# Performance work log

Measured on AMD Instinct MI355X. Metric: run time of the kernel, lower is better.

## Reference

```python
import jax, jax.numpy as jnp
import numpy as np

N_NODES = 100000
N_EDGES = 3200000
IN_DIM = 256
OUT_DIM = 128


def setup_inputs() -> dict:
    key = jax.random.key(0)
    k_x, k_w, k_r, k_c, k_v = jax.random.split(key, 5)
    X = jax.random.normal(k_x, (N_NODES, IN_DIM), dtype=jnp.float32)
    # kaiming_normal on [in, out]: fan computed along dim 1 -> std = sqrt(2/out)
    weight = jax.random.normal(k_w, (IN_DIM, OUT_DIM), dtype=jnp.float32) * np.sqrt(2.0 / OUT_DIM)
    bias = jnp.zeros((OUT_DIM,), dtype=jnp.float32)
    adj_rows = jax.random.randint(k_r, (N_EDGES,), 0, N_NODES, dtype=jnp.int32)
    adj_cols = jax.random.randint(k_c, (N_EDGES,), 0, N_NODES, dtype=jnp.int32)
    adj_vals = jax.random.uniform(k_v, (N_EDGES,), dtype=jnp.float32)
    return {"X": X, "weight": weight, "bias": bias,
            "adj_rows": adj_rows, "adj_cols": adj_cols, "adj_vals": adj_vals}


def reference(X, weight, bias, adj_rows, adj_cols, adj_vals):
    # support = X @ W  -> [N, out]
    support = jnp.matmul(X, weight)
    # SpMM: output[r] = sum_e vals[e] * support[cols[e]] for edges with rows[e]==r
    messages = adj_vals[:, None] * support[adj_cols]          # [E, out]
    output = jax.ops.segment_sum(messages, adj_rows, num_segments=N_NODES)
    return output + bias
```

## Files before the change

### kernel.cpp

```cpp
#include <hip/hip_runtime.h>

#define N_NODES 100000
#define N_EDGES 3200000
#define IN_DIM  256
#define OUT_DIM 128

#define CB      256
#define NCB     391
#define NB2     256
#define CHUNK2  12500
#define NQ4     (CHUNK2 / 4)
#define SCAN_N  (NCB * NB2)
#define SCAN_BS 1024
#define SCAN_NB ((SCAN_N + SCAN_BS - 1) / SCAN_BS)

#define GBM 128

typedef __attribute__((ext_vector_type(8))) short bf16x8;
typedef __attribute__((ext_vector_type(4))) float f32x4;
typedef unsigned int u32x2 __attribute__((ext_vector_type(2)));
typedef unsigned int u32x4 __attribute__((ext_vector_type(4)));

__device__ __forceinline__ unsigned short f2bf(float x) {
    unsigned u = __float_as_uint(x);
    unsigned r = (u + 0x7FFFu + ((u >> 16) & 1u)) >> 16;
    return (unsigned short)r;
}
__device__ __forceinline__ unsigned cvtpk_bf16(float lo, float hi) {
    unsigned r;
    asm("v_cvt_pk_bf16_f32 %0, %1, %2" : "=v"(r) : "v"(lo), "v"(hi));
    return r;
}
__device__ __forceinline__ float bflo(unsigned d) { return __uint_as_float(d << 16); }
__device__ __forceinline__ float bfhi(unsigned d) { return __uint_as_float(d & 0xFFFF0000u); }

__global__ __launch_bounds__(256) void wtrans_kernel(const float* __restrict__ W,
                                                     unsigned short* __restrict__ WT) {
    const int n = blockIdx.x;
    const int k = threadIdx.x;
    WT[(size_t)n * IN_DIM + k] = f2bf(W[(size_t)k * OUT_DIM + n]);
}

__global__ __launch_bounds__(256) void gemm_mfma(const float* __restrict__ X,
                                                 const unsigned short* __restrict__ WT,
                                                 unsigned short* __restrict__ SH) {
    __shared__ char lds[32768];
    char* ldsX = lds;
    char* ldsW = lds + 16384;

    const int t    = threadIdx.x;
    const int row0 = blockIdx.x * GBM;
    const int w    = t >> 6;
    const int l    = t & 63;
    const int r16  = l & 15;
    const int kg   = l >> 4;

    f32x4 acc[2][8];
#pragma unroll
    for (int mr = 0; mr < 2; ++mr)
#pragma unroll
        for (int nc = 0; nc < 8; ++nc) acc[mr][nc] = (f32x4)(0.f);

    const int srow = t >> 1;
    const int sseg = t & 1;

    for (int k0 = 0; k0 < IN_DIM; k0 += 64) {
        {
            int grow = row0 + srow;
            bool live = grow < N_NODES;
            const float4* xp = (const float4*)(X + (size_t)(live ? grow : 0) * IN_DIM + k0 + sseg * 32);
#pragma unroll
            for (int c = 0; c < 4; ++c) {
                uint4 wv = make_uint4(0, 0, 0, 0);
                if (live) {
                    float4 fa = xp[c * 2], fb = xp[c * 2 + 1];
                    wv.x = cvtpk_bf16(fa.x, fa.y);
                    wv.y = cvtpk_bf16(fa.z, fa.w);
                    wv.z = cvtpk_bf16(fb.x, fb.y);
                    wv.w = cvtpk_bf16(fb.z, fb.w);
                }
                int byte = srow * 128 + (sseg * 32 + c * 8) * 2;
                byte ^= (srow & 7) << 4;
                *(uint4*)(ldsX + byte) = wv;
            }
            const uint4* wp = (const uint4*)(WT + (size_t)srow * IN_DIM + k0 + sseg * 32);
#pragma unroll
            for (int c = 0; c < 4; ++c) {
                uint4 wv = wp[c];
                int byte = srow * 128 + (sseg * 32 + c * 8) * 2;
                byte ^= (srow & 7) << 4;
                *(uint4*)(ldsW + byte) = wv;
            }
        }
        __syncthreads();

#pragma unroll
        for (int ks = 0; ks < 64; ks += 32) {
            bf16x8 af[2], bfr[8];
#pragma unroll
            for (int mr = 0; mr < 2; ++mr) {
                int row  = w * 32 + mr * 16 + r16;
                int byte = row * 128 + (ks + kg * 8) * 2;
                byte ^= (row & 7) << 4;
                af[mr] = *(const bf16x8*)(ldsX + byte);
            }
#pragma unroll
            for (int nc = 0; nc < 8; ++nc) {
                int n    = nc * 16 + r16;
                int byte = n * 128 + (ks + kg * 8) * 2;
                byte ^= (n & 7) << 4;
                bfr[nc] = *(const bf16x8*)(ldsW + byte);
            }
#pragma unroll
            for (int mr = 0; mr < 2; ++mr)
#pragma unroll
                for (int nc = 0; nc < 8; ++nc)
                    acc[mr][nc] = __builtin_amdgcn_mfma_f32_16x16x32_bf16(af[mr], bfr[nc], acc[mr][nc], 0, 0, 0);
        }
        __syncthreads();
    }

#pragma unroll
    for (int mr = 0; mr < 2; ++mr)
#pragma unroll
        for (int j = 0; j < 4; ++j) {
            int grow = row0 + w * 32 + mr * 16 + kg * 4 + j;
            if (grow < N_NODES) {
#pragma unroll
                for (int nc = 0; nc < 8; ++nc)
                    SH[(size_t)grow * OUT_DIM + nc * 16 + r16] = f2bf(acc[mr][nc][j]);
            }
        }
}

__global__ __launch_bounds__(1024) void pA_hist(const int* __restrict__ rows,
                                                int* __restrict__ gcounts) {
    __shared__ int hist[NCB];
    const int b = blockIdx.x, t = threadIdx.x;
    for (int k = t; k < NCB; k += 1024) hist[k] = 0;
    __syncthreads();
    const int4* r4 = (const int4*)(rows + b * CHUNK2);
    for (int q = t; q < NQ4; q += 1024) {
        int4 r = r4[q];
        atomicAdd(&hist[r.x >> 8], 1);
        atomicAdd(&hist[r.y >> 8], 1);
        atomicAdd(&hist[r.z >> 8], 1);
        atomicAdd(&hist[r.w >> 8], 1);
    }
    __syncthreads();
    for (int k = t; k < NCB; k += 1024) gcounts[k * NB2 + b] = hist[k];
}

__global__ __launch_bounds__(256) void scan1_kernel(int* __restrict__ data,
                                                    int* __restrict__ bsums) {
    __shared__ int tsum[256];
    const int t    = threadIdx.x;
    const int base = blockIdx.x * SCAN_BS + t * 4;
    int v[4];
#pragma unroll
    for (int j = 0; j < 4; ++j) {
        int idx = base + j;
        v[j] = (idx < SCAN_N) ? data[idx] : 0;
    }
    tsum[t] = v[0] + v[1] + v[2] + v[3];
    __syncthreads();
    for (int off = 1; off < 256; off <<= 1) {
        int x = (t >= off) ? tsum[t - off] : 0;
        __syncthreads();
        tsum[t] += x;
        __syncthreads();
    }
    int run = (t == 0) ? 0 : tsum[t - 1];
#pragma unroll
    for (int j = 0; j < 4; ++j) {
        int idx = base + j;
        if (idx < SCAN_N) data[idx] = run;
        run += v[j];
    }
    if (t == 255) bsums[blockIdx.x] = tsum[255];
}

__global__ __launch_bounds__(64) void scan2_kernel(int* __restrict__ bsums) {
    const int lane = threadIdx.x & 63;
    const int base = lane * 4;
    int v[4];
    int s = 0;
#pragma unroll
    for (int j = 0; j < 4; ++j) {
        int idx = base + j;
        v[j] = (idx < SCAN_NB) ? bsums[idx] : 0;
        s += v[j];
    }
    for (int off = 1; off < 64; off <<= 1) {
        int x = __shfl_up(s, off);
        if (lane >= off) s += x;
    }
    int run = s - v[0] - v[1] - v[2] - v[3];
#pragma unroll
    for (int j = 0; j < 4; ++j) {
        int idx = base + j;
        if (idx < SCAN_NB) bsums[idx] = run;
        run += v[j];
    }
}

__global__ __launch_bounds__(256) void scan3_kernel(int* __restrict__ data,
                                                    const int* __restrict__ bsums) {
    int i = blockIdx.x * 256 + threadIdx.x;
    if (i < SCAN_N) data[i] += bsums[i / SCAN_BS];
}

__global__ __launch_bounds__(1024) void pA_scatter(const int* __restrict__ rows,
                                                   const int* __restrict__ cols,
                                                   const float* __restrict__ vals,
                                                   const int* __restrict__ pscan,
                                                   uint2* __restrict__ sorted) {
    __shared__ int cursor[NCB];
    const int b = blockIdx.x, t = threadIdx.x;
    for (int k = t; k < NCB; k += 1024) cursor[k] = pscan[k * NB2 + b];
    __syncthreads();
    const int4*   r4 = (const int4*)(rows + b * CHUNK2);
    const int4*   c4 = (const int4*)(cols + b * CHUNK2);
    const float4* v4 = (const float4*)(vals + b * CHUNK2);
    for (int q = t; q < NQ4; q += 1024) {
        int4   r = r4[q];
        int4   c = c4[q];
        float4 v = v4[q];
#define PUT(rr, cc, vv)                                                        \
        {                                                                      \
            int pos = atomicAdd(&cursor[(rr) >> 8], 1);                        \
            sorted[pos] = make_uint2(__float_as_uint(vv),                      \
                                     ((unsigned)((rr) & (CB - 1)) << 17) | (unsigned)(cc)); \
        }
        PUT(r.x, c.x, v.x)
        PUT(r.y, c.y, v.y)
        PUT(r.z, c.z, v.z)
        PUT(r.w, c.w, v.w)
#undef PUT
    }
}

__global__ __launch_bounds__(1024) void pB_sort(const uint2* __restrict__ sortedA,
                                                const int* __restrict__ pscan,
                                                unsigned* __restrict__ sorted2,
                                                int* __restrict__ rstart2) {
    __shared__ int cnt[CB];
    __shared__ int cur[CB];
    __shared__ int sbuf[2][CB];
    const int cb = blockIdx.x, t = threadIdx.x;
    const int beg  = pscan[cb * NB2];
    const int gend = (cb == NCB - 1) ? N_EDGES : pscan[(cb + 1) * NB2];

    if (t < CB) cnt[t] = 0;
    __syncthreads();

    for (int i = beg + t; i < gend; i += 1024)
        atomicAdd(&cnt[(sortedA[i].y >> 17) & (CB - 1)], 1);
    __syncthreads();

    if (t < CB) sbuf[0][t] = cnt[t];
    __syncthreads();
    int p = 0;
    for (int off = 1; off < CB; off <<= 1) {
        if (t < CB) sbuf[p ^ 1][t] = sbuf[p][t] + ((t >= off) ? sbuf[p][t - off] : 0);
        __syncthreads();
        p ^= 1;
    }
    if (t < CB) {
        int excl = (t == 0) ? 0 : sbuf[p][t - 1];
        int gi   = cb * CB + t;
        if (gi <= N_NODES) rstart2[gi] = beg + excl;
        cur[t] = beg + excl;
    }
    __syncthreads();

    for (int i = beg + t; i < gend; i += 1024) {
        uint2 m  = sortedA[i];
        int   rl = (int)((m.y >> 17) & (CB - 1));
        int  pos = atomicAdd(&cur[rl], 1);
        float v  = __uint_as_float(m.x);
        unsigned vq = (unsigned)__float2int_rn(v * 32767.0f);
        sorted2[pos] = (m.y & 0x1FFFFu) | (vq << 17);
    }
}

__global__ __launch_bounds__(256) void p6_rowsum(const int* __restrict__ rstart2,
                                                 const unsigned* __restrict__ meta,
                                                 const unsigned short* __restrict__ SH,
                                                 const float* __restrict__ bias,
                                                 float* __restrict__ out) {
    const int wid  = (blockIdx.x * 256 + threadIdx.x) >> 6;
    const int lane = threadIdx.x & 63;
    if (wid >= N_NODES) return;

    const int beg = rstart2[wid];
    const int end = rstart2[wid + 1];
    const int qg  = lane >> 4;
    const int ql  = lane & 15;

    float a0 = 0.f, a1 = 0.f, a2 = 0.f, a3 = 0.f, a4 = 0.f, a5 = 0.f, a6 = 0.f, a7 = 0.f;

#define DEQ(mm) ((float)((mm) >> 17) * (1.0f / 32767.0f))
#define GATHER(mm) (*((const u32x4*)(SH + (size_t)((mm) & 0x1FFFFu) * OUT_DIM) + ql))
#define ACC8(vv, gg)                                          \
    {                                                         \
        a0 += (vv) * bflo((gg).x); a1 += (vv) * bfhi((gg).x); \
        a2 += (vv) * bflo((gg).y); a3 += (vv) * bfhi((gg).y); \
        a4 += (vv) * bflo((gg).z); a5 += (vv) * bfhi((gg).z); \
        a6 += (vv) * bflo((gg).w); a7 += (vv) * bfhi((gg).w); \
    }

    int i = beg;
    for (; i + 8 <= end; i += 8) {
        unsigned m0 = meta[i + qg];
        unsigned m1 = meta[i + 4 + qg];
        u32x4 g0 = GATHER(m0);
        u32x4 g1 = GATHER(m1);
        float v0 = DEQ(m0);
        float v1 = DEQ(m1);
        ACC8(v0, g0)
        ACC8(v1, g1)
    }
    for (; i < end; i += 4) {
        int      idx  = i + qg;
        int      cidx = (idx < end) ? idx : (end - 1);
        unsigned m    = meta[cidx];
        float    v    = (idx < end) ? DEQ(m) : 0.f;
        u32x4    g    = GATHER(m);
        ACC8(v, g)
    }
#undef ACC8
#undef GATHER
#undef DEQ

    a0 += __shfl_xor(a0, 16); a1 += __shfl_xor(a1, 16); a2 += __shfl_xor(a2, 16); a3 += __shfl_xor(a3, 16);
    a4 += __shfl_xor(a4, 16); a5 += __shfl_xor(a5, 16); a6 += __shfl_xor(a6, 16); a7 += __shfl_xor(a7, 16);
    a0 += __shfl_xor(a0, 32); a1 += __shfl_xor(a1, 32); a2 += __shfl_xor(a2, 32); a3 += __shfl_xor(a3, 32);
    a4 += __shfl_xor(a4, 32); a5 += __shfl_xor(a5, 32); a6 += __shfl_xor(a6, 32); a7 += __shfl_xor(a7, 32);

    if (lane < 16) {
        const float4* bp = (const float4*)bias + ql * 2;
        float4 b0 = bp[0], b1 = bp[1];
        f32x4 o0 = {a0 + b0.x, a1 + b0.y, a2 + b0.z, a3 + b0.w};
        f32x4 o1 = {a4 + b1.x, a5 + b1.y, a6 + b1.z, a7 + b1.w};
        f32x4* orow = (f32x4*)(out + (size_t)wid * OUT_DIM) + ql * 2;
        __builtin_nontemporal_store(o0, orow);
        __builtin_nontemporal_store(o1, orow + 1);
    }
}

extern "C" void kernel_launch(void* const* d_in, const int* in_sizes, int n_in,
                              void* d_out, int out_size, void* d_ws, size_t ws_size,
                              hipStream_t stream) {
    const float* X    = (const float*)d_in[0];
    const float* W    = (const float*)d_in[1];
    const float* bias = (const float*)d_in[2];
    const int*   rows = (const int*)d_in[3];
    const int*   cols = (const int*)d_in[4];
    const float* vals = (const float*)d_in[5];
    float* out = (float*)d_out;

    char* ws = (char*)d_ws;
    unsigned short* SH      = (unsigned short*)ws;
    uint2*          sortedA = (uint2*)(ws + 25600000);
    unsigned*       sorted2 = (unsigned*)(ws + 51200000);
    int*            pscan   = (int*)(ws + 64000000);
    int*            rstart2 = (int*)(ws + 64400384);
    int*            bsums   = (int*)(ws + 64800768);
    unsigned short* WT      = (unsigned short*)(ws + 64801280);

    hipLaunchKernelGGL(wtrans_kernel, dim3(OUT_DIM), dim3(IN_DIM), 0, stream, W, WT);
    hipLaunchKernelGGL(gemm_mfma, dim3((N_NODES + GBM - 1) / GBM), dim3(256), 0, stream,
                       X, WT, SH);
    hipLaunchKernelGGL(pA_hist, dim3(NB2), dim3(1024), 0, stream, rows, pscan);
    hipLaunchKernelGGL(scan1_kernel, dim3(SCAN_NB), dim3(256), 0, stream, pscan, bsums);
    hipLaunchKernelGGL(scan2_kernel, dim3(1), dim3(64), 0, stream, bsums);
    hipLaunchKernelGGL(scan3_kernel, dim3((SCAN_N + 255) / 256), dim3(256), 0, stream,
                       pscan, bsums);
    hipLaunchKernelGGL(pA_scatter, dim3(NB2), dim3(1024), 0, stream,
                       rows, cols, vals, pscan, sortedA);
    hipLaunchKernelGGL(pB_sort, dim3(NCB), dim3(1024), 0, stream,
                       sortedA, pscan, sorted2, rstart2);
    hipLaunchKernelGGL(p6_rowsum, dim3((N_NODES + 3) / 4), dim3(256), 0, stream,
                       rstart2, sorted2, SH, bias, out);
}
```

Measured before the change: 201.6 us.

## Compute per-row counts in histogram pass and prefetch metadata in rowsum

The histogram kernel now also builds a per-row edge count with global atomics, so the second-stage sort no longer rereads all of sortedA to count rows. The rowsum gather loop is restructured to software-prefetch the next metadata words before doing the current gathers. The cost is 3.2M extra global atomics on a 100k-entry array plus an extra zeroing kernel launch, which could offset the saved pass over sortedA.

```diff
diff --git a/kernel.cpp b/kernel.cpp
--- a/kernel.cpp
+++ b/kernel.cpp
@@ -39,6 +39,11 @@
     const int n = blockIdx.x;
     const int k = threadIdx.x;
     WT[(size_t)n * IN_DIM + k] = f2bf(W[(size_t)k * OUT_DIM + n]);
+}
+
+__global__ __launch_bounds__(256) void zero_rowcnt(int* __restrict__ rowcnt) {
+    int i = blockIdx.x * 256 + threadIdx.x;
+    if (i < SCAN_N) rowcnt[i] = 0;
 }
 
 __global__ __launch_bounds__(256) void gemm_mfma(const float* __restrict__ X,
@@ -134,7 +139,8 @@
 }
 
 __global__ __launch_bounds__(1024) void pA_hist(const int* __restrict__ rows,
-                                                int* __restrict__ gcounts) {
+                                                int* __restrict__ gcounts,
+                                                int* __restrict__ rowcnt) {
     __shared__ int hist[NCB];
     const int b = blockIdx.x, t = threadIdx.x;
     for (int k = t; k < NCB; k += 1024) hist[k] = 0;
@@ -146,6 +152,10 @@
         atomicAdd(&hist[r.y >> 8], 1);
         atomicAdd(&hist[r.z >> 8], 1);
         atomicAdd(&hist[r.w >> 8], 1);
+        atomicAdd(&rowcnt[r.x], 1);
+        atomicAdd(&rowcnt[r.y], 1);
+        atomicAdd(&rowcnt[r.z], 1);
+        atomicAdd(&rowcnt[r.w], 1);
     }
     __syncthreads();
     for (int k = t; k < NCB; k += 1024) gcounts[k * NB2 + b] = hist[k];
@@ -242,23 +252,19 @@
 
 __global__ __launch_bounds__(1024) void pB_sort(const uint2* __restrict__ sortedA,
                                                 const int* __restrict__ pscan,
+                                                const int* __restrict__ rowcnt,
                                                 unsigned* __restrict__ sorted2,
                                                 int* __restrict__ rstart2) {
-    __shared__ int cnt[CB];
     __shared__ int cur[CB];
     __shared__ int sbuf[2][CB];
     const int cb = blockIdx.x, t = threadIdx.x;
     const int beg  = pscan[cb * NB2];
     const int gend = (cb == NCB - 1) ? N_EDGES : pscan[(cb + 1) * NB2];
 
-    if (t < CB) cnt[t] = 0;
-    __syncthreads();
-
-    for (int i = beg + t; i < gend; i += 1024)
-        atomicAdd(&cnt[(sortedA[i].y >> 17) & (CB - 1)], 1);
-    __syncthreads();
-
-    if (t < CB) sbuf[0][t] = cnt[t];
+    if (t < CB) {
+        int gi = cb * CB + t;
+        sbuf[0][t] = (gi < N_NODES) ? rowcnt[gi] : 0;
+    }
     __syncthreads();
     int p = 0;
     for (int off = 1; off < CB; off <<= 1) {
@@ -311,15 +317,31 @@
     }
 
     int i = beg;
-    for (; i + 8 <= end; i += 8) {
-        unsigned m0 = meta[i + qg];
-        unsigned m1 = meta[i + 4 + qg];
-        u32x4 g0 = GATHER(m0);
-        u32x4 g1 = GATHER(m1);
-        float v0 = DEQ(m0);
-        float v1 = DEQ(m1);
+    unsigned pm0 = 0, pm1 = 0;
+    if (i + 8 <= end) {
+        pm0 = meta[i + qg];
+        pm1 = meta[i + 4 + qg];
+    }
+    for (; i + 16 <= end; i += 8) {
+        unsigned nm0 = meta[i + 8 + qg];
+        unsigned nm1 = meta[i + 12 + qg];
+        u32x4 g0 = GATHER(pm0);
+        u32x4 g1 = GATHER(pm1);
+        float v0 = DEQ(pm0);
+        float v1 = DEQ(pm1);
         ACC8(v0, g0)
         ACC8(v1, g1)
+        pm0 = nm0;
+        pm1 = nm1;
+    }
+    if (i + 8 <= end) {
+        u32x4 g0 = GATHER(pm0);
+        u32x4 g1 = GATHER(pm1);
+        float v0 = DEQ(pm0);
+        float v1 = DEQ(pm1);
+        ACC8(v0, g0)
+        ACC8(v1, g1)
+        i += 8;
     }
     for (; i < end; i += 4) {
         int      idx  = i + qg;
@@ -366,13 +388,15 @@
     unsigned*       sorted2 = (unsigned*)(ws + 51200000);
     int*            pscan   = (int*)(ws + 64000000);
     int*            rstart2 = (int*)(ws + 64400384);
-    int*            bsums   = (int*)(ws + 64800768);
-    unsigned short* WT      = (unsigned short*)(ws + 64801280);
-
+    int*            rowcnt  = (int*)(ws + 64800768);
+    int*            bsums   = (int*)(ws + 65201152);
+    unsigned short* WT      = (unsigned short*)(ws + 65201664);
+
+    hipLaunchKernelGGL(zero_rowcnt, dim3((SCAN_N + 255) / 256), dim3(256), 0, stream, rowcnt);
     hipLaunchKernelGGL(wtrans_kernel, dim3(OUT_DIM), dim3(IN_DIM), 0, stream, W, WT);
     hipLaunchKernelGGL(gemm_mfma, dim3((N_NODES + GBM - 1) / GBM), dim3(256), 0, stream,
                        X, WT, SH);
-    hipLaunchKernelGGL(pA_hist, dim3(NB2), dim3(1024), 0, stream, rows, pscan);
+    hipLaunchKernelGGL(pA_hist, dim3(NB2), dim3(1024), 0, stream, rows, pscan, rowcnt);
     hipLaunchKernelGGL(scan1_kernel, dim3(SCAN_NB), dim3(256), 0, stream, pscan, bsums);
     hipLaunchKernelGGL(scan2_kernel, dim3(1), dim3(64), 0, stream, bsums);
     hipLaunchKernelGGL(scan3_kernel, dim3((SCAN_N + 255) / 256), dim3(256), 0, stream,
@@ -380,7 +404,7 @@
     hipLaunchKernelGGL(pA_scatter, dim3(NB2), dim3(1024), 0, stream,
                        rows, cols, vals, pscan, sortedA);
     hipLaunchKernelGGL(pB_sort, dim3(NCB), dim3(1024), 0, stream,
-                       sortedA, pscan, sorted2, rstart2);
+                       sortedA, pscan, rowcnt, sorted2, rstart2);
     hipLaunchKernelGGL(p6_rowsum, dim3((N_NODES + 3) / 4), dim3(256), 0, stream,
                        rstart2, sorted2, SH, bias, out);
 }
```

Measured after the change: 323.5 us. 60.4% more time.

## Replace LDS-staged GEMM with direct global-to-register MFMA fragment loads

Applied to the files above, without the earlier changes.

Rewrites the dense X@W GEMM so each wavefront loads its A fragments from X and its B fragments from the transposed bf16 weight directly into registers, with no LDS staging or __syncthreads. Blocks grow to 512 threads (8 waves of 32 rows each) and the grid is sized to NCB blocks. This removes LDS traffic and barrier stalls, but every wave now reloads the full weight matrix from global/L2 and the A loads are less coalesced (16 rows per fragment, 32-byte segments).

```diff
diff --git a/kernel.cpp b/kernel.cpp
--- a/kernel.cpp
+++ b/kernel.cpp
@@ -14,12 +14,12 @@
 #define SCAN_BS 1024
 #define SCAN_NB ((SCAN_N + SCAN_BS - 1) / SCAN_BS)
 
-#define GBM 128
-
 typedef __attribute__((ext_vector_type(8))) short bf16x8;
 typedef __attribute__((ext_vector_type(4))) float f32x4;
 typedef unsigned int u32x2 __attribute__((ext_vector_type(2)));
 typedef unsigned int u32x4 __attribute__((ext_vector_type(4)));
+
+union pkcast { u32x4 u; bf16x8 h; };
 
 __device__ __forceinline__ unsigned short f2bf(float x) {
     unsigned u = __float_as_uint(x);
@@ -41,94 +41,53 @@
     WT[(size_t)n * IN_DIM + k] = f2bf(W[(size_t)k * OUT_DIM + n]);
 }
 
-__global__ __launch_bounds__(256) void gemm_mfma(const float* __restrict__ X,
-                                                 const unsigned short* __restrict__ WT,
-                                                 unsigned short* __restrict__ SH) {
-    __shared__ char lds[32768];
-    char* ldsX = lds;
-    char* ldsW = lds + 16384;
-
+__global__ __launch_bounds__(512) void gemm_direct(const float* __restrict__ X,
+                                                   const unsigned short* __restrict__ WT,
+                                                   unsigned short* __restrict__ SH) {
     const int t    = threadIdx.x;
-    const int row0 = blockIdx.x * GBM;
     const int w    = t >> 6;
     const int l    = t & 63;
     const int r16  = l & 15;
     const int kg   = l >> 4;
+    const int row0 = (blockIdx.x * 8 + w) * 32;
 
     f32x4 acc[2][8];
 #pragma unroll
-    for (int mr = 0; mr < 2; ++mr)
-#pragma unroll
-        for (int nc = 0; nc < 8; ++nc) acc[mr][nc] = (f32x4)(0.f);
-
-    const int srow = t >> 1;
-    const int sseg = t & 1;
-
-    for (int k0 = 0; k0 < IN_DIM; k0 += 64) {
-        {
-            int grow = row0 + srow;
-            bool live = grow < N_NODES;
-            const float4* xp = (const float4*)(X + (size_t)(live ? grow : 0) * IN_DIM + k0 + sseg * 32);
-#pragma unroll
-            for (int c = 0; c < 4; ++c) {
-                uint4 wv = make_uint4(0, 0, 0, 0);
-                if (live) {
-                    float4 fa = xp[c * 2], fb = xp[c * 2 + 1];
-                    wv.x = cvtpk_bf16(fa.x, fa.y);
-                    wv.y = cvtpk_bf16(fa.z, fa.w);
-                    wv.z = cvtpk_bf16(fb.x, fb.y);
-                    wv.w = cvtpk_bf16(fb.z, fb.w);
-                }
-                int byte = srow * 128 + (sseg * 32 + c * 8) * 2;
-                byte ^= (srow & 7) << 4;
-                *(uint4*)(ldsX + byte) = wv;
-            }
-            const uint4* wp = (const uint4*)(WT + (size_t)srow * IN_DIM + k0 + sseg * 32);
-#pragma unroll
-            for (int c = 0; c < 4; ++c) {
-                uint4 wv = wp[c];
-                int byte = srow * 128 + (sseg * 32 + c * 8) * 2;
-                byte ^= (srow & 7) << 4;
-                *(uint4*)(ldsW + byte) = wv;
-            }
+    for (int m = 0; m < 2; ++m)
+#pragma unroll
+        for (int nc = 0; nc < 8; ++nc) acc[m][nc] = (f32x4)(0.f);
+
+#pragma unroll
+    for (int k0 = 0; k0 < IN_DIM; k0 += 32) {
+        bf16x8 af[2];
+#pragma unroll
+        for (int m = 0; m < 2; ++m) {
+            int row = row0 + m * 16 + r16;
+            if (row >= N_NODES) row = N_NODES - 1;
+            const float4* ap = (const float4*)(X + (size_t)row * IN_DIM + k0 + kg * 8);
+            float4 fa = ap[0], fb = ap[1];
+            pkcast pc;
+            pc.u = (u32x4){cvtpk_bf16(fa.x, fa.y), cvtpk_bf16(fa.z, fa.w),
+                           cvtpk_bf16(fb.x, fb.y), cvtpk_bf16(fb.z, fb.w)};
+            af[m] = pc.h;
         }
-        __syncthreads();
-
-#pragma unroll
-        for (int ks = 0; ks < 64; ks += 32) {
-            bf16x8 af[2], bfr[8];
-#pragma unroll
-            for (int mr = 0; mr < 2; ++mr) {
-                int row  = w * 32 + mr * 16 + r16;
-                int byte = row * 128 + (ks + kg * 8) * 2;
-                byte ^= (row & 7) << 4;
-                af[mr] = *(const bf16x8*)(ldsX + byte);
-            }
-#pragma unroll
-            for (int nc = 0; nc < 8; ++nc) {
-                int n    = nc * 16 + r16;
-                int byte = n * 128 + (ks + kg * 8) * 2;
-                byte ^= (n & 7) << 4;
-                bfr[nc] = *(const bf16x8*)(ldsW + byte);
-            }
-#pragma unroll
-            for (int mr = 0; mr < 2; ++mr)
+#pragma unroll
+        for (int nc = 0; nc < 8; ++nc) {
+            bf16x8 bfrag = *(const bf16x8*)(WT + (size_t)(nc * 16 + r16) * IN_DIM + k0 + kg * 8);
+            acc[0][nc] = __builtin_amdgcn_mfma_f32_16x16x32_bf16(af[0], bfrag, acc[0][nc], 0, 0, 0);
+            acc[1][nc] = __builtin_amdgcn_mfma_f32_16x16x32_bf16(af[1], bfrag, acc[1][nc], 0, 0, 0);
+        }
+    }
+
+#pragma unroll
+    for (int m = 0; m < 2; ++m)
+#pragma unroll
+        for (int j = 0; j < 4; ++j) {
+            int row = row0 + m * 16 + kg * 4 + j;
+            if (row < N_NODES) {
 #pragma unroll
                 for (int nc = 0; nc < 8; ++nc)
-                    acc[mr][nc] = __builtin_amdgcn_mfma_f32_16x16x32_bf16(af[mr], bfr[nc], acc[mr][nc], 0, 0, 0);
-        }
-        __syncthreads();
-    }
-
-#pragma unroll
-    for (int mr = 0; mr < 2; ++mr)
-#pragma unroll
-        for (int j = 0; j < 4; ++j) {
-            int grow = row0 + w * 32 + mr * 16 + kg * 4 + j;
-            if (grow < N_NODES) {
-#pragma unroll
-                for (int nc = 0; nc < 8; ++nc)
-                    SH[(size_t)grow * OUT_DIM + nc * 16 + r16] = f2bf(acc[mr][nc][j]);
+                    SH[(size_t)row * OUT_DIM + nc * 16 + r16] = f2bf(acc[m][nc][j]);
             }
         }
 }
@@ -370,8 +329,7 @@
     unsigned short* WT      = (unsigned short*)(ws + 64801280);
 
     hipLaunchKernelGGL(wtrans_kernel, dim3(OUT_DIM), dim3(IN_DIM), 0, stream, W, WT);
-    hipLaunchKernelGGL(gemm_mfma, dim3((N_NODES + GBM - 1) / GBM), dim3(256), 0, stream,
-                       X, WT, SH);
+    hipLaunchKernelGGL(gemm_direct, dim3(NCB), dim3(512), 0, stream, X, WT, SH);
     hipLaunchKernelGGL(pA_hist, dim3(NB2), dim3(1024), 0, stream, rows, pscan);
     hipLaunchKernelGGL(scan1_kernel, dim3(SCAN_NB), dim3(256), 0, stream, pscan, bsums);
     hipLaunchKernelGGL(scan2_kernel, dim3(1), dim3(64), 0, stream, bsums);
```

Result: slower. 217.7 us (+8.0%).

## Pack edges into 32-bit words with 8-bit values and stage pB sort in LDS

Applied to the files above, without the earlier changes.

The first scatter pass now writes one packed 32-bit word per edge (8-bit quantized value, 7-bit local row, 17-bit column) instead of an 8-byte pair, which halves intermediate traffic. Coarse buckets shrink from 256 to 128 rows and the bucket count doubles. The second sort pass caches the bucket's edges in LDS during the counting pass, so the scatter pass reads them from LDS instead of re-reading global memory. The cost is coarser value quantization (8-bit instead of 15-bit), which may exceed the accuracy tolerance, and a larger prefix scan.

```diff
diff --git a/kernel.cpp b/kernel.cpp
--- a/kernel.cpp
+++ b/kernel.cpp
@@ -5,20 +5,20 @@
 #define IN_DIM  256
 #define OUT_DIM 128
 
-#define CB      256
-#define NCB     391
+#define CB      128
+#define NCB     782
 #define NB2     256
 #define CHUNK2  12500
 #define NQ4     (CHUNK2 / 4)
 #define SCAN_N  (NCB * NB2)
 #define SCAN_BS 1024
 #define SCAN_NB ((SCAN_N + SCAN_BS - 1) / SCAN_BS)
+#define LDSE    4864
 
 #define GBM 128
 
 typedef __attribute__((ext_vector_type(8))) short bf16x8;
 typedef __attribute__((ext_vector_type(4))) float f32x4;
-typedef unsigned int u32x2 __attribute__((ext_vector_type(2)));
 typedef unsigned int u32x4 __attribute__((ext_vector_type(4)));
 
 __device__ __forceinline__ unsigned short f2bf(float x) {
@@ -142,10 +142,10 @@
     const int4* r4 = (const int4*)(rows + b * CHUNK2);
     for (int q = t; q < NQ4; q += 1024) {
         int4 r = r4[q];
-        atomicAdd(&hist[r.x >> 8], 1);
-        atomicAdd(&hist[r.y >> 8], 1);
-        atomicAdd(&hist[r.z >> 8], 1);
-        atomicAdd(&hist[r.w >> 8], 1);
+        atomicAdd(&hist[r.x >> 7], 1);
+        atomicAdd(&hist[r.y >> 7], 1);
+        atomicAdd(&hist[r.z >> 7], 1);
+        atomicAdd(&hist[r.w >> 7], 1);
     }
     __syncthreads();
     for (int k = t; k < NCB; k += 1024) gcounts[k * NB2 + b] = hist[k];
@@ -214,7 +214,7 @@
                                                    const int* __restrict__ cols,
                                                    const float* __restrict__ vals,
                                                    const int* __restrict__ pscan,
-                                                   uint2* __restrict__ sorted) {
+                                                   unsigned* __restrict__ mraw) {
     __shared__ int cursor[NCB];
     const int b = blockIdx.x, t = threadIdx.x;
     for (int k = t; k < NCB; k += 1024) cursor[k] = pscan[k * NB2 + b];
@@ -228,9 +228,9 @@
         float4 v = v4[q];
 #define PUT(rr, cc, vv)                                                        \
         {                                                                      \
-            int pos = atomicAdd(&cursor[(rr) >> 8], 1);                        \
-            sorted[pos] = make_uint2(__float_as_uint(vv),                      \
-                                     ((unsigned)((rr) & (CB - 1)) << 17) | (unsigned)(cc)); \
+            int pos = atomicAdd(&cursor[(rr) >> 7], 1);                        \
+            unsigned vq = (unsigned)__float2int_rn((vv) * 255.0f);             \
+            mraw[pos] = (vq << 24) | ((unsigned)((rr) & (CB - 1)) << 17) | (unsigned)(cc); \
         }
         PUT(r.x, c.x, v.x)
         PUT(r.y, c.y, v.y)
@@ -240,22 +240,28 @@
     }
 }
 
-__global__ __launch_bounds__(1024) void pB_sort(const uint2* __restrict__ sortedA,
+__global__ __launch_bounds__(1024) void pB_sort(const unsigned* __restrict__ mraw,
                                                 const int* __restrict__ pscan,
                                                 unsigned* __restrict__ sorted2,
                                                 int* __restrict__ rstart2) {
+    __shared__ unsigned ebuf[LDSE];
     __shared__ int cnt[CB];
     __shared__ int cur[CB];
     __shared__ int sbuf[2][CB];
     const int cb = blockIdx.x, t = threadIdx.x;
     const int beg  = pscan[cb * NB2];
     const int gend = (cb == NCB - 1) ? N_EDGES : pscan[(cb + 1) * NB2];
+    const int n    = gend - beg;
+    const int nl   = (n < LDSE) ? n : LDSE;
 
     if (t < CB) cnt[t] = 0;
     __syncthreads();
 
-    for (int i = beg + t; i < gend; i += 1024)
-        atomicAdd(&cnt[(sortedA[i].y >> 17) & (CB - 1)], 1);
+    for (int i = t; i < n; i += 1024) {
+        unsigned m = mraw[beg + i];
+        if (i < LDSE) ebuf[i] = m;
+        atomicAdd(&cnt[(m >> 17) & (CB - 1)], 1);
+    }
     __syncthreads();
 
     if (t < CB) sbuf[0][t] = cnt[t];
@@ -274,13 +280,17 @@
     }
     __syncthreads();
 
-    for (int i = beg + t; i < gend; i += 1024) {
-        uint2 m  = sortedA[i];
-        int   rl = (int)((m.y >> 17) & (CB - 1));
-        int  pos = atomicAdd(&cur[rl], 1);
-        float v  = __uint_as_float(m.x);
-        unsigned vq = (unsigned)__float2int_rn(v * 32767.0f);
-        sorted2[pos] = (m.y & 0x1FFFFu) | (vq << 17);
+    for (int i = t; i < nl; i += 1024) {
+        unsigned m = ebuf[i];
+        int rl  = (int)((m >> 17) & (CB - 1));
+        int pos = atomicAdd(&cur[rl], 1);
+        sorted2[pos] = m;
+    }
+    for (int i = nl + t; i < n; i += 1024) {
+        unsigned m = mraw[beg + i];
+        int rl  = (int)((m >> 17) & (CB - 1));
+        int pos = atomicAdd(&cur[rl], 1);
+        sorted2[pos] = m;
     }
 }
 
@@ -300,7 +310,7 @@
 
     float a0 = 0.f, a1 = 0.f, a2 = 0.f, a3 = 0.f, a4 = 0.f, a5 = 0.f, a6 = 0.f, a7 = 0.f;
 
-#define DEQ(mm) ((float)((mm) >> 17) * (1.0f / 32767.0f))
+#define DEQ(mm) ((float)((mm) >> 24) * (1.0f / 255.0f))
 #define GATHER(mm) (*((const u32x4*)(SH + (size_t)((mm) & 0x1FFFFu) * OUT_DIM) + ql))
 #define ACC8(vv, gg)                                          \
     {                                                         \
@@ -362,12 +372,12 @@
 
     char* ws = (char*)d_ws;
     unsigned short* SH      = (unsigned short*)ws;
-    uint2*          sortedA = (uint2*)(ws + 25600000);
-    unsigned*       sorted2 = (unsigned*)(ws + 51200000);
-    int*            pscan   = (int*)(ws + 64000000);
-    int*            rstart2 = (int*)(ws + 64400384);
-    int*            bsums   = (int*)(ws + 64800768);
-    unsigned short* WT      = (unsigned short*)(ws + 64801280);
+    unsigned*       mraw    = (unsigned*)(ws + 25600000);
+    unsigned*       sorted2 = (unsigned*)(ws + 38400000);
+    int*            pscan   = (int*)(ws + 51200000);
+    int*            rstart2 = (int*)(ws + 52000768);
+    int*            bsums   = (int*)(ws + 52401152);
+    unsigned short* WT      = (unsigned short*)(ws + 52402176);
 
     hipLaunchKernelGGL(wtrans_kernel, dim3(OUT_DIM), dim3(IN_DIM), 0, stream, W, WT);
     hipLaunchKernelGGL(gemm_mfma, dim3((N_NODES + GBM - 1) / GBM), dim3(256), 0, stream,
@@ -378,9 +388,9 @@
     hipLaunchKernelGGL(scan3_kernel, dim3((SCAN_N + 255) / 256), dim3(256), 0, stream,
                        pscan, bsums);
     hipLaunchKernelGGL(pA_scatter, dim3(NB2), dim3(1024), 0, stream,
-                       rows, cols, vals, pscan, sortedA);
+                       rows, cols, vals, pscan, mraw);
     hipLaunchKernelGGL(pB_sort, dim3(NCB), dim3(1024), 0, stream,
-                       sortedA, pscan, sorted2, rstart2);
+                       mraw, pscan, sorted2, rstart2);
     hipLaunchKernelGGL(p6_rowsum, dim3((N_NODES + 3) / 4), dim3(256), 0, stream,
                        rstart2, sorted2, SH, bias, out);
 }
```

New measurement: 203.4 us. Within noise of the previous version (+0.9%).
